# Optimization experiments

Hardware: AMD Instinct MI355X
Metric: run time of the kernel (lower is better)

Reference implementation:

```python
import jax, jax.numpy as jnp
import numpy as np

D = 768      # qkv.in_features (ViT-Base)
R = 16       # LoRA rank
T = 8        # task_id: number of previously saved adapters
B_, S_ = 32, 256
TAU = 1.0


def setup_inputs() -> dict:
    key = jax.random.key(0)
    ks = jax.random.split(key, 13)
    s = lambda k, shape, sc=0.02: jax.random.normal(k, shape, jnp.float32) * sc
    return {
        "x": jax.random.normal(ks[0], (B_, S_, D), jnp.float32),
        "qkv_w": s(ks[1], (3 * D, D)),           # torch Linear weight [out,in]
        "qkv_b": s(ks[2], (3 * D,)),
        "la_q": s(ks[3], (R, D)),                # current-task LoRA A_q [r,d]
        "lb_q": s(ks[4], (D, R)),                # current-task LoRA B_q [d,r]
        "la_v": s(ks[5], (R, D)),
        "lb_v": s(ks[6], (D, R)),
        "A_q": s(ks[7], (T, R, D)),              # saved per-task A_q stacks
        "B_q": s(ks[8], (T, D, R)),
        "A_v": s(ks[9], (T, R, D)),
        "B_v": s(ks[10], (T, D, R)),
        "gate_logits": jax.random.normal(ks[11], (T,), jnp.float32),
        "alpha": jnp.ones((T + 1,), jnp.float32),  # gumbel_gate.alpha, indexed by task_id
    }


def _moe_branch(x, A, B, beta):
    """Weighted sum over T tasks of (x @ A_t^T @ B_t^T) / (||A_t||*||B_t||), weight beta_t.

    Vectorizes the per-task serial low-rank matmuls of the torch loop into two
    batched einsums; beta/norm scaling is folded into B to avoid materializing
    per-task [B,S,D] outputs.
    """
    nA = jnp.sqrt(jnp.sum(A * A, axis=(1, 2)))   # [T] Frobenius norms
    nB = jnp.sqrt(jnp.sum(B * B, axis=(1, 2)))
    scale = beta / (nA * nB)                      # [T]
    za = jnp.einsum('bsd,trd->bstr', x, A)       # [B,S,T,r]
    Bs = B * scale[:, None, None]                 # [T,D,r]
    return jnp.einsum('bstr,tdr->bsd', za, Bs)   # [B,S,D]


def _lora(x, a, b):
    # torch: b(a(x)) with Linear weights a:[r,d], b:[d,r]
    return jnp.einsum('bsr,dr->bsd', jnp.einsum('bsd,rd->bsr', x, a), b)


def reference(x, qkv_w, qkv_b, la_q, lb_q, la_v, lb_v, A_q, B_q, A_v, B_v, gate_logits, alpha):
    # Gumbel-softmax gate over tasks (deterministic/eval path: softmax(logits/tau), hard=False)
    beta = jax.nn.softmax(gate_logits / TAU)
    a_cur = alpha[T]  # alpha[self.task_id]
    new_q = _moe_branch(x, A_q, B_q, beta) + a_cur * _lora(x, la_q, lb_q)
    new_v = _moe_branch(x, A_v, B_v, beta) + a_cur * _lora(x, la_v, lb_v)
    qkv = jnp.einsum('bsd,ed->bse', x, qkv_w) + qkv_b  # [B,S,3D]
    qkv = qkv.at[..., :D].add(new_q)
    qkv = qkv.at[..., 2 * D:].add(new_v)
    return qkv
```

## Files before the change

kernel.cpp:

```cpp
#include <hip/hip_runtime.h>

#define TOK 8192
#define DD  768
#define NOUT 2304
#define TT  8
#define RR  16
#define KRANK 144

typedef __bf16 bf16;
typedef __bf16 bf16x4 __attribute__((ext_vector_type(4)));
typedef __bf16 bf16x8 __attribute__((ext_vector_type(8)));
typedef float  floatx4 __attribute__((ext_vector_type(4)));

__device__ __forceinline__ void gl_lds16(const void* g, void* l) {
    __builtin_amdgcn_global_load_lds((const __attribute__((address_space(1))) void*)g,
                                     (__attribute__((address_space(3))) void*)l, 16, 0, 0);
}

__global__ __launch_bounds__(256) void prep_kernel(
    const float* __restrict__ A_q, const float* __restrict__ B_q,
    const float* __restrict__ A_v, const float* __restrict__ B_v,
    const float* __restrict__ x, bf16* __restrict__ xb,
    float* __restrict__ norms)
{
    __shared__ float ws4[4];
    const int b = blockIdx.x;
    if (b < 32) {
        const float* base;
        switch (b >> 3) {
            case 0: base = A_q; break;
            case 1: base = B_q; break;
            case 2: base = A_v; break;
            default: base = B_v; break;
        }
        base += (b & 7) * (RR * DD);
        float s = 0.f;
        for (int i = threadIdx.x; i < RR * DD; i += 256) {
            float v = base[i];
            s = fmaf(v, v, s);
        }
        #pragma unroll
        for (int off = 32; off > 0; off >>= 1) s += __shfl_down(s, off);
        if ((threadIdx.x & 63) == 0) ws4[threadIdx.x >> 6] = s;
        __syncthreads();
        if (threadIdx.x == 0)
            norms[b] = sqrtf(ws4[0] + ws4[1] + ws4[2] + ws4[3]);
    } else {
        const int idx = ((b - 32) * 256 + threadIdx.x) * 8;
        const float4 v0 = *(const float4*)(x + idx);
        const float4 v1 = *(const float4*)(x + idx + 4);
        bf16x8 o = { (bf16)v0.x, (bf16)v0.y, (bf16)v0.z, (bf16)v0.w,
                     (bf16)v1.x, (bf16)v1.y, (bf16)v1.z, (bf16)v1.w };
        *(bf16x8*)(xb + idx) = o;
    }
}

__global__ __launch_bounds__(256) void fold_kernel(
    const float* __restrict__ qkv_w,
    const float* __restrict__ A_q, const float* __restrict__ la_q,
    const float* __restrict__ B_q, const float* __restrict__ lb_q,
    const float* __restrict__ A_v, const float* __restrict__ la_v,
    const float* __restrict__ B_v, const float* __restrict__ lb_v,
    const float* __restrict__ gate_logits, const float* __restrict__ alpha,
    const float* __restrict__ norms, bf16* __restrict__ Wc)
{
    const int tid = threadIdx.x;
    const int d = blockIdx.x * 256 + tid;
    const int gy = blockIdx.y;

    if (gy >= 96 && gy < 192) {
        const int rowbase = DD + (gy - 96) * 8;
        #pragma unroll
        for (int j = 0; j < 8; ++j) {
            const int row = rowbase + j;
            Wc[row * DD + d] = (bf16)qkv_w[row * DD + d];
        }
        return;
    }

    __shared__ float c_lds[8 * KRANK];
    __shared__ float sc_sh[TT];
    __shared__ float acur_sh;

    const bool is_v = (gy >= 192);
    const int e0 = (is_v ? gy - 192 : gy) * 8;
    const float* Astack = is_v ? A_v : A_q;
    const float* la     = is_v ? la_v : la_q;
    const float* Bmat   = is_v ? B_v : B_q;
    const float* lb     = is_v ? lb_v : lb_q;
    const float* nA     = norms + (is_v ? 16 : 0);
    const float* nB     = norms + (is_v ? 24 : 8);
    const int rowbase   = (is_v ? 2 * DD : 0) + e0;

    if (tid == 0) {
        float mx = gate_logits[0];
        for (int t = 1; t < TT; ++t) mx = fmaxf(mx, gate_logits[t]);
        float e[TT], s = 0.f;
        for (int t = 0; t < TT; ++t) { e[t] = __expf(gate_logits[t] - mx); s += e[t]; }
        for (int t = 0; t < TT; ++t) sc_sh[t] = (e[t] / s) / (nA[t] * nB[t]);
        acur_sh = alpha[TT];
    }
    __syncthreads();

    for (int idx = tid; idx < 8 * KRANK; idx += 256) {
        const int j = idx / KRANK, i = idx - j * KRANK;
        const int e = e0 + j;
        float v;
        if (i < TT * RR) {
            const int t = i >> 4, r = i & 15;
            v = sc_sh[t] * Bmat[(t * DD + e) * RR + r];
        } else {
            v = acur_sh * lb[e * RR + (i - TT * RR)];
        }
        c_lds[j * KRANK + i] = v;
    }
    __syncthreads();

    float acc[8] = {0.f, 0.f, 0.f, 0.f, 0.f, 0.f, 0.f, 0.f};

    for (int i = 0; i < TT * RR; i += 4) {
        const float a0 = Astack[(i + 0) * DD + d];
        const float a1 = Astack[(i + 1) * DD + d];
        const float a2 = Astack[(i + 2) * DD + d];
        const float a3 = Astack[(i + 3) * DD + d];
        #pragma unroll
        for (int j = 0; j < 8; ++j) {
            const float4 cv = *(const float4*)&c_lds[j * KRANK + i];
            acc[j] = fmaf(a0, cv.x, fmaf(a1, cv.y, fmaf(a2, cv.z, fmaf(a3, cv.w, acc[j]))));
        }
    }
    #pragma unroll
    for (int i = 0; i < RR; i += 4) {
        const float a0 = la[(i + 0) * DD + d];
        const float a1 = la[(i + 1) * DD + d];
        const float a2 = la[(i + 2) * DD + d];
        const float a3 = la[(i + 3) * DD + d];
        #pragma unroll
        for (int j = 0; j < 8; ++j) {
            const float4 cv = *(const float4*)&c_lds[j * KRANK + TT * RR + i];
            acc[j] = fmaf(a0, cv.x, fmaf(a1, cv.y, fmaf(a2, cv.z, fmaf(a3, cv.w, acc[j]))));
        }
    }

    #pragma unroll
    for (int j = 0; j < 8; ++j) {
        const int row = rowbase + j;
        Wc[row * DD + d] = (bf16)(qkv_w[row * DD + d] + acc[j]);
    }
}

__global__ __launch_bounds__(256, 2) void gemm_kernel(
    const bf16* __restrict__ A, const bf16* __restrict__ B,
    const float* __restrict__ bias, float* __restrict__ C)
{
    __shared__ __align__(16) char smem[69632];
    bf16* const lds_a = (bf16*)smem;
    bf16* const lds_b = (bf16*)(smem + 32768);

    const int tid  = threadIdx.x;
    const int lane = tid & 63;
    const int wave = tid >> 6;

    const int flat  = blockIdx.x;
    const int xcd   = flat & 7;
    const int local = flat >> 3;
    const int mb    = xcd * 8 + (local & 7);
    const int nb    = local >> 3;
    const int m0 = mb * 128;
    const int n0 = nb * 144;

    const int wm = wave * 32;

    const int srow = lane >> 3;
    const int scol = ((lane & 7) ^ srow) * 8;

    floatx4 acc[2][9];
    #pragma unroll
    for (int i = 0; i < 2; ++i)
        #pragma unroll
        for (int j = 0; j < 9; ++j)
            acc[i][j] = (floatx4){0.f, 0.f, 0.f, 0.f};

    const bf16* const gA = A + (m0 + srow) * DD + scol;
    const bf16* const gB = B + (n0 + srow) * DD + scol;

    auto stage = [&](int buf, int k0) {
        bf16* la = lds_a + buf * (128 * 64);
        bf16* lb = lds_b + buf * (144 * 64);
        for (int c = wave; c < 34; c += 4) {
            if (c < 16) gl_lds16(gA + c * 8 * DD + k0, la + c * 512);
            else        gl_lds16(gB + (c - 16) * 8 * DD + k0, lb + (c - 16) * 512);
        }
    };

    stage(0, 0);

    for (int kt = 0; kt < 12; ++kt) {
        const int cur = kt & 1;
        if (kt < 11) {
            stage(cur ^ 1, (kt + 1) * 64);
            asm volatile("s_waitcnt vmcnt(8)" ::: "memory");
        } else {
            asm volatile("s_waitcnt vmcnt(0)" ::: "memory");
        }
        __builtin_amdgcn_s_barrier();
        asm volatile("" ::: "memory");

        const bf16* la = lds_a + cur * (128 * 64);
        const bf16* lb = lds_b + cur * (144 * 64);
        #pragma unroll
        for (int ks = 0; ks < 2; ++ks) {
            const int c_log = ks * 4 + (lane >> 4);
            bf16x8 af[2];
            #pragma unroll
            for (int mt = 0; mt < 2; ++mt) {
                const int r = wm + mt * 16 + (lane & 15);
                af[mt] = *(const bf16x8*)&la[r * 64 + ((c_log ^ (r & 7)) * 8)];
            }
            #pragma unroll
            for (int nt = 0; nt < 9; ++nt) {
                const int r = nt * 16 + (lane & 15);
                const bf16x8 bfr = *(const bf16x8*)&lb[r * 64 + ((c_log ^ (r & 7)) * 8)];
                #pragma unroll
                for (int mt = 0; mt < 2; ++mt)
                    acc[mt][nt] = __builtin_amdgcn_mfma_f32_16x16x32_bf16(
                        af[mt], bfr, acc[mt][nt], 0, 0, 0);
            }
        }
        asm volatile("" ::: "memory");
        __builtin_amdgcn_s_barrier();
    }

    const int cr = (lane >> 4) * 4;
    const int cc = lane & 15;
    #pragma unroll
    for (int nt = 0; nt < 9; ++nt) {
        const int gn = n0 + nt * 16 + cc;
        const float bv = bias[gn];
        #pragma unroll
        for (int mt = 0; mt < 2; ++mt) {
            const int gm = m0 + wm + mt * 16 + cr;
            #pragma unroll
            for (int r = 0; r < 4; ++r)
                C[(gm + r) * NOUT + gn] = acc[mt][nt][r] + bv;
        }
    }
}

extern "C" void kernel_launch(void* const* d_in, const int* in_sizes, int n_in,
                              void* d_out, int out_size, void* d_ws, size_t ws_size,
                              hipStream_t stream)
{
    const float* x           = (const float*)d_in[0];
    const float* qkv_w       = (const float*)d_in[1];
    const float* qkv_b       = (const float*)d_in[2];
    const float* la_q        = (const float*)d_in[3];
    const float* lb_q        = (const float*)d_in[4];
    const float* la_v        = (const float*)d_in[5];
    const float* lb_v        = (const float*)d_in[6];
    const float* A_q         = (const float*)d_in[7];
    const float* B_q         = (const float*)d_in[8];
    const float* A_v         = (const float*)d_in[9];
    const float* B_v         = (const float*)d_in[10];
    const float* gate_logits = (const float*)d_in[11];
    const float* alpha       = (const float*)d_in[12];
    float* out = (float*)d_out;

    char* ws = (char*)d_ws;
    bf16*  Xbf    = (bf16*)ws;
    bf16*  Wc     = (bf16*)(ws + 12582912);
    float* norms  = (float*)(ws + 12582912 + 3538944);

    prep_kernel<<<32 + TOK * DD / 2048, 256, 0, stream>>>(A_q, B_q, A_v, B_v,
                                                          x, Xbf, norms);
    fold_kernel<<<dim3(3, 288), 256, 0, stream>>>(qkv_w,
                                                  A_q, la_q, B_q, lb_q,
                                                  A_v, la_v, B_v, lb_v,
                                                  gate_logits, alpha, norms, Wc);
    gemm_kernel<<<1024, 256, 0, stream>>>(Xbf, Wc, qkv_b, out);
}
```

Before: 176.8 us.

## Widen GEMM tile to 128x288 with 8 waves and triple-buffered LDS pipeline

The GEMM block now uses 512 threads (8 waves arranged 4x2) and computes a 128x288 output tile, halving the grid to 512 blocks. LDS staging moves from double to triple buffering with a prefetch distance of two k-tiles. This removes the second barrier per iteration, and MFMA sections are wrapped in s_setprio to favour compute waves. The aim is more reuse of each A tile and better overlap of global-to-LDS loads with MFMA. In exchange, the kernel needs about 156 KB of LDS, which allows only one block per CU and reduces latency hiding across blocks.

```diff
diff --git a/kernel.cpp b/kernel.cpp
--- a/kernel.cpp
+++ b/kernel.cpp
@@ -149,13 +149,11 @@
     }
 }
 
-__global__ __launch_bounds__(256, 2) void gemm_kernel(
+__global__ __launch_bounds__(512, 2) void gemm_kernel(
     const bf16* __restrict__ A, const bf16* __restrict__ B,
     const float* __restrict__ bias, float* __restrict__ C)
 {
-    __shared__ __align__(16) char smem[69632];
-    bf16* const lds_a = (bf16*)smem;
-    bf16* const lds_b = (bf16*)(smem + 32768);
+    __shared__ __align__(16) char smem[159744];
 
     const int tid  = threadIdx.x;
     const int lane = tid & 63;
@@ -167,9 +165,10 @@
     const int mb    = xcd * 8 + (local & 7);
     const int nb    = local >> 3;
     const int m0 = mb * 128;
-    const int n0 = nb * 144;
-
-    const int wm = wave * 32;
+    const int n0 = nb * 288;
+
+    const int wm = (wave >> 1) * 32;
+    const int wn = (wave & 1) * 144;
 
     const int srow = lane >> 3;
     const int scol = ((lane & 7) ^ srow) * 8;
@@ -184,30 +183,34 @@
     const bf16* const gA = A + (m0 + srow) * DD + scol;
     const bf16* const gB = B + (n0 + srow) * DD + scol;
 
-    auto stage = [&](int buf, int k0) {
-        bf16* la = lds_a + buf * (128 * 64);
-        bf16* lb = lds_b + buf * (144 * 64);
-        for (int c = wave; c < 34; c += 4) {
+    auto stage = [&](int buf, int kt) {
+        bf16* la = (bf16*)(smem + buf * 53248);
+        bf16* lb = (bf16*)(smem + buf * 53248 + 16384);
+        const int k0 = kt * 64;
+        for (int c = wave; c < 52; c += 8) {
             if (c < 16) gl_lds16(gA + c * 8 * DD + k0, la + c * 512);
             else        gl_lds16(gB + (c - 16) * 8 * DD + k0, lb + (c - 16) * 512);
         }
     };
 
     stage(0, 0);
+    stage(1, 1);
 
     for (int kt = 0; kt < 12; ++kt) {
-        const int cur = kt & 1;
         if (kt < 11) {
-            stage(cur ^ 1, (kt + 1) * 64);
-            asm volatile("s_waitcnt vmcnt(8)" ::: "memory");
+            asm volatile("s_waitcnt vmcnt(6)" ::: "memory");
         } else {
             asm volatile("s_waitcnt vmcnt(0)" ::: "memory");
         }
         __builtin_amdgcn_s_barrier();
         asm volatile("" ::: "memory");
 
-        const bf16* la = lds_a + cur * (128 * 64);
-        const bf16* lb = lds_b + cur * (144 * 64);
+        if (kt < 10) stage((kt + 2) % 3, kt + 2);
+
+        const bf16* la = (bf16*)(smem + (kt % 3) * 53248);
+        const bf16* lb = (bf16*)(smem + (kt % 3) * 53248 + 16384);
+
+        __builtin_amdgcn_s_setprio(1);
         #pragma unroll
         for (int ks = 0; ks < 2; ++ks) {
             const int c_log = ks * 4 + (lane >> 4);
@@ -219,7 +222,7 @@
             }
             #pragma unroll
             for (int nt = 0; nt < 9; ++nt) {
-                const int r = nt * 16 + (lane & 15);
+                const int r = wn + nt * 16 + (lane & 15);
                 const bf16x8 bfr = *(const bf16x8*)&lb[r * 64 + ((c_log ^ (r & 7)) * 8)];
                 #pragma unroll
                 for (int mt = 0; mt < 2; ++mt)
@@ -227,22 +230,22 @@
                         af[mt], bfr, acc[mt][nt], 0, 0, 0);
             }
         }
+        __builtin_amdgcn_s_setprio(0);
         asm volatile("" ::: "memory");
-        __builtin_amdgcn_s_barrier();
     }
 
     const int cr = (lane >> 4) * 4;
     const int cc = lane & 15;
     #pragma unroll
     for (int nt = 0; nt < 9; ++nt) {
-        const int gn = n0 + nt * 16 + cc;
+        const int gn = n0 + wn + nt * 16 + cc;
         const float bv = bias[gn];
         #pragma unroll
         for (int mt = 0; mt < 2; ++mt) {
-            const int gm = m0 + wm + mt * 16 + cr;
+            const int gmb = m0 + wm + mt * 16 + cr;
             #pragma unroll
             for (int r = 0; r < 4; ++r)
-                C[(gm + r) * NOUT + gn] = acc[mt][nt][r] + bv;
+                C[(gmb + r) * NOUT + gn] = acc[mt][nt][r] + bv;
         }
     }
 }
@@ -277,5 +280,5 @@
                                                   A_q, la_q, B_q, lb_q,
                                                   A_v, la_v, B_v, lb_v,
                                                   gate_logits, alpha, norms, Wc);
-    gemm_kernel<<<1024, 256, 0, stream>>>(Xbf, Wc, qkv_b, out);
-}
+    gemm_kernel<<<512, 512, 0, stream>>>(Xbf, Wc, qkv_b, out);
+}
```

New measurement: 177.9 us. No clear change (+0.7%).
